# Kernel tuning notes

Hardware: AMD Instinct MI355X
Metric: run time of the kernel (lower is better)

Reference implementation:

```python
import jax, jax.numpy as jnp
import numpy as np

DIM = 1024
H = 16
HD = DIM // H  # 64
B, N = 2, 2048
EPS = 1e-6


def setup_inputs() -> dict:
    key = jax.random.key(0)
    ks = jax.random.split(key, 12)
    s = 0.02
    return {
        "x": jax.random.normal(ks[0], (B, N, DIM), jnp.float32),
        "rotary_cos": jax.random.uniform(ks[1], (B, N, HD), jnp.float32),
        "rotary_sin": jax.random.uniform(ks[2], (B, N, HD), jnp.float32),
        "Wq": jax.random.normal(ks[3], (DIM, DIM), jnp.float32) * s,
        "bq": jnp.zeros((DIM,), jnp.float32),
        "Wk": jax.random.normal(ks[4], (DIM, DIM), jnp.float32) * s,
        "bk": jnp.zeros((DIM,), jnp.float32),
        "Wv": jax.random.normal(ks[5], (DIM, DIM), jnp.float32) * s,
        "bv": jnp.zeros((DIM,), jnp.float32),
        "q_norm_w": jnp.ones((HD,), jnp.float32),
        "q_norm_b": jnp.zeros((HD,), jnp.float32),
        "k_norm_w": jnp.ones((HD,), jnp.float32),
        "k_norm_b": jnp.zeros((HD,), jnp.float32),
        "Wo": jax.random.normal(ks[6], (DIM, DIM), jnp.float32) * s,
        "bo": jnp.zeros((DIM,), jnp.float32),
    }


def _layernorm(x, w, b):
    mu = jnp.mean(x, axis=-1, keepdims=True)
    var = jnp.mean(jnp.square(x - mu), axis=-1, keepdims=True)
    return (x - mu) * jax.lax.rsqrt(var + EPS) * w + b


def _rotate_half(x):
    x1, x2 = jnp.split(x, 2, axis=-1)
    return jnp.concatenate((-x2, x1), axis=-1)


def _apply_rope(x, cos, sin):
    # x: [B,H,N,D]; cos/sin: [B,N,D] -> [B,1,N,D]
    cos = cos[:, None]
    sin = sin[:, None]
    return x * cos + _rotate_half(x) * sin


def reference(x, rotary_cos, rotary_sin, Wq, bq, Wk, bk, Wv, bv,
              q_norm_w, q_norm_b, k_norm_w, k_norm_b, Wo, bo):
    b, n, c = x.shape
    q = x @ Wq + bq
    k = x @ Wk + bk
    v = x @ Wv + bv
    # Faithful packed-qkv permutation: cat -> view(.., H, 3*hd) -> split(hd)
    qkv = jnp.concatenate((q, k, v), axis=-1).reshape(b, n, H, 3 * HD)
    q, k, v = jnp.split(qkv, 3, axis=-1)  # each [B,N,H,HD]
    q = q.transpose(0, 2, 1, 3)  # [B,H,N,HD]
    k = k.transpose(0, 2, 1, 3)
    v = v.transpose(0, 2, 1, 3)
    q = _layernorm(q, q_norm_w, q_norm_b)
    k = _layernorm(k, k_norm_w, k_norm_b)
    q = _apply_rope(q, rotary_cos, rotary_sin)
    k = _apply_rope(k, rotary_cos, rotary_sin)
    scale = HD ** -0.5
    scores = jnp.einsum("bhqd,bhkd->bhqk", q, k) * scale
    probs = jax.nn.softmax(scores, axis=-1)
    out = jnp.einsum("bhqk,bhkd->bhqd", probs, v)
    out = out.transpose(0, 2, 1, 3).reshape(b, n, c)
    return out @ Wo + bo
```

## Files before the change

### kernel.cpp

```cpp
#include <hip/hip_runtime.h>

typedef __attribute__((ext_vector_type(8))) __bf16 bf16x8;
typedef __attribute__((ext_vector_type(4))) float  f32x4;

#define DEV __device__ __forceinline__

DEV void async_copy16(const void* g, void* l) {
  __builtin_amdgcn_global_load_lds((const __attribute__((address_space(1))) void*)g,
                                   (__attribute__((address_space(3))) void*)l, 16, 0, 0);
}

DEV float ldf(const void* p, size_t i, int isbf) {
  if (isbf) {
    unsigned int w = ((unsigned int)((const unsigned short*)p)[i]) << 16;
    float f; __builtin_memcpy(&f, &w, 4); return f;
  }
  return ((const float*)p)[i];
}

__global__ void detect_dtype(const unsigned short* __restrict__ x, int* __restrict__ flag) {
  int bad = 0;
#pragma unroll
  for (int i = 0; i < 4; i++) {
    unsigned short u = x[threadIdx.x + i * 64];
    int e = (u >> 7) & 0xFF;
    if (e >= 0x90) bad = 1;
  }
  int anybad = __any(bad);
  if (threadIdx.x == 0) flag[0] = anybad ? 0 : 1;
}

__global__ __launch_bounds__(256) void prep(const void* __restrict__ Wq,
                                            const void* __restrict__ Wk,
                                            const void* __restrict__ Wv,
                                            const void* __restrict__ Wo,
                                            const void* __restrict__ x,
                                            const void* __restrict__ bq,
                                            const void* __restrict__ bk,
                                            const void* __restrict__ bv,
                                            const void* __restrict__ bo,
                                            const int* __restrict__ flag,
                                            __bf16* __restrict__ Wt,
                                            __bf16* __restrict__ Wot,
                                            __bf16* __restrict__ x_bf,
                                            float* __restrict__ bias) {
  __shared__ float tile[32][33];
  const int isbf = flag[0];
  const int tid = threadIdx.x;
  const int z = blockIdx.z;

  if (z < 4) {
    const void* in = (z == 0) ? Wq : (z == 1) ? Wk : (z == 2) ? Wv : Wo;
    __bf16* out = (z < 3) ? (Wt + (size_t)z * 1024 * 1024) : Wot;
    const int tx = tid & 31, ty = tid >> 5;
    const int r0 = blockIdx.y * 32, c0 = blockIdx.x * 32;
#pragma unroll
    for (int i = 0; i < 4; i++) {
      int r = ty + i * 8;
      tile[r][tx] = ldf(in, (size_t)(r0 + r) * 1024 + c0 + tx, isbf);
    }
    __syncthreads();
#pragma unroll
    for (int i = 0; i < 4; i++) {
      int r = ty + i * 8;
      out[(size_t)(c0 + r) * 1024 + r0 + tx] = (__bf16)tile[tx][r];
    }
  } else {
    const int id = blockIdx.y * 32 + blockIdx.x;
    if (isbf) {
#pragma unroll
      for (int j = 0; j < 4; j++) {
        int idx = id * 1024 + j * 256 + tid;
        ((uint2*)x_bf)[idx] = ((const uint2*)x)[idx];
      }
    } else {
#pragma unroll
      for (int j = 0; j < 4; j++) {
        int idx = id * 1024 + j * 256 + tid;
        float4 f = ((const float4*)x)[idx];
        union { __bf16 h[4]; uint2 u; } pk;
        pk.h[0] = (__bf16)f.x; pk.h[1] = (__bf16)f.y;
        pk.h[2] = (__bf16)f.z; pk.h[3] = (__bf16)f.w;
        ((uint2*)x_bf)[idx] = pk.u;
      }
    }
    if (id < 16) {
      int i = id * 256 + tid;
      if (i < 1024)      bias[i] = ldf(bq, i, isbf);
      else if (i < 2048) bias[i] = ldf(bk, i - 1024, isbf);
      else if (i < 3072) bias[i] = ldf(bv, i - 2048, isbf);
      else               bias[i] = ldf(bo, i - 3072, isbf);
    }
  }
}

template <int DYN>
__global__ __launch_bounds__(256, 2) void gemm_bt(const __bf16* __restrict__ A,
                                                  const __bf16* __restrict__ Bt,
                                                  const float* __restrict__ bias,
                                                  void* __restrict__ Cout,
                                                  const int* __restrict__ flag,
                                                  int M, int N, int K) {
  __shared__ __align__(16) __bf16 As[128 * 64];
  __shared__ __align__(16) __bf16 Bs[128 * 64];
  const int tid = threadIdx.x;
  const int wid = tid >> 6, lane = tid & 63;
  const int m_blk = blockIdx.x * 128, n_blk = blockIdx.y * 128;
  const int wm = (wid & 1) * 64, wn = (wid >> 1) * 64;
  const int l8 = lane >> 3, l7 = lane & 7;
  const int cc = l7 ^ (l8 & 7);
  const int q4 = lane >> 4, l15 = lane & 15;

  f32x4 acc[4][4] = {};

  for (int kb = 0; kb < K; kb += 64) {
    __syncthreads();
#pragma unroll
    for (int i = 0; i < 4; i++) {
      int row = i * 32 + wid * 8 + l8;
      async_copy16(A + (size_t)(m_blk + row) * K + kb + cc * 8,
                   As + (i * 32 + wid * 8) * 64);
      async_copy16(Bt + (size_t)(n_blk + row) * K + kb + cc * 8,
                   Bs + (i * 32 + wid * 8) * 64);
    }
    __syncthreads();
#pragma unroll
    for (int k0 = 0; k0 < 64; k0 += 32) {
      bf16x8 a[4], b[4];
#pragma unroll
      for (int i = 0; i < 4; i++) {
        int ra = wm + i * 16 + l15;
        int ba = ra * 8 + (((k0 >> 3) + q4) ^ (ra & 7));
        a[i] = *(const bf16x8*)&As[ba * 8];
        int rb = wn + i * 16 + l15;
        int bb = rb * 8 + (((k0 >> 3) + q4) ^ (rb & 7));
        b[i] = *(const bf16x8*)&Bs[bb * 8];
      }
#pragma unroll
      for (int i = 0; i < 4; i++)
#pragma unroll
        for (int j = 0; j < 4; j++)
          acc[i][j] = __builtin_amdgcn_mfma_f32_16x16x32_bf16(a[i], b[j], acc[i][j], 0, 0, 0);
    }
  }

  const int isbf = DYN ? flag[0] : 1;
  float bcol[4];
#pragma unroll
  for (int j = 0; j < 4; j++) bcol[j] = bias[n_blk + wn + j * 16 + l15];
#pragma unroll
  for (int i = 0; i < 4; i++)
#pragma unroll
    for (int j = 0; j < 4; j++) {
      int col = n_blk + wn + j * 16 + l15;
#pragma unroll
      for (int r = 0; r < 4; r++) {
        int row = m_blk + wm + i * 16 + q4 * 4 + r;
        float v = acc[i][j][r] + bcol[j];
        size_t idx = (size_t)row * N + col;
        if (isbf) ((__bf16*)Cout)[idx] = (__bf16)v;
        else      ((float*)Cout)[idx] = v;
      }
    }
}

__global__ __launch_bounds__(256) void ln_rope_v(const __bf16* __restrict__ qkv,
                                                 const void* __restrict__ rcos,
                                                 const void* __restrict__ rsin,
                                                 const void* __restrict__ qw,
                                                 const void* __restrict__ qb,
                                                 const void* __restrict__ kw,
                                                 const void* __restrict__ kb_,
                                                 const int* __restrict__ flag,
                                                 __bf16* __restrict__ Qp,
                                                 __bf16* __restrict__ Kp,
                                                 __bf16* __restrict__ Vt) {
  __shared__ __bf16 vt[64][68];
  const int isbf = flag[0];
  const int tid = threadIdx.x, w = tid >> 6, lane = tid & 63;
  const int bh = blockIdx.y, h = bh & 15, b = bh >> 4;
  const int n0 = blockIdx.x * 64;

  float gq = ldf(qw, lane, isbf), bq_ = ldf(qb, lane, isbf);
  float gk = ldf(kw, lane, isbf), bk_ = ldf(kb_, lane, isbf);

  for (int t = 0; t < 16; t++) {
    const int n = n0 + w * 16 + t;
    const size_t tok = (size_t)b * 2048 + n;
    const __bf16* base = qkv + tok * 3072 + h * 192;
    float qv = (float)base[lane], kv = (float)base[64 + lane], vv = (float)base[128 + lane];

    float sq = qv, sk = kv;
#pragma unroll
    for (int m = 1; m < 64; m <<= 1) { sq += __shfl_xor(sq, m, 64); sk += __shfl_xor(sk, m, 64); }
    float muq = sq * (1.0f / 64.0f), muk = sk * (1.0f / 64.0f);
    float tq = qv - muq, tk = kv - muk;
    float vq = tq * tq, vk = tk * tk;
#pragma unroll
    for (int m = 1; m < 64; m <<= 1) { vq += __shfl_xor(vq, m, 64); vk += __shfl_xor(vk, m, 64); }
    float rsq = rsqrtf(vq * (1.0f / 64.0f) + 1e-6f);
    float rsk = rsqrtf(vk * (1.0f / 64.0f) + 1e-6f);
    float qn = tq * rsq * gq + bq_;
    float kn = tk * rsk * gk + bk_;

    float c = ldf(rcos, tok * 64 + lane, isbf), s = ldf(rsin, tok * 64 + lane, isbf);
    float qpart = __shfl_xor(qn, 32, 64), kpart = __shfl_xor(kn, 32, 64);
    float qrh = (lane < 32) ? -qpart : qpart;
    float krh = (lane < 32) ? -kpart : kpart;

    const size_t oidx = ((size_t)bh * 2048 + n) * 64 + lane;
    Qp[oidx] = (__bf16)((qn * c + qrh * s) * 0.1803368801111204f);
    Kp[oidx] = (__bf16)(kn * c + krh * s);
    vt[lane][w * 16 + t] = (__bf16)vv;
  }
  __syncthreads();
  const int row = tid >> 2, qt = tid & 3;
  size_t gbase = (size_t)bh * 64 * 2048 + (size_t)row * 2048 + n0 + qt * 16;
#pragma unroll
  for (int u = 0; u < 4; u++)
    *(uint2*)&Vt[gbase + u * 4] = *(const uint2*)&vt[row][qt * 16 + u * 4];
}

__global__ __launch_bounds__(256, 2) void attn(const __bf16* __restrict__ Qp,
                                               const __bf16* __restrict__ Kp,
                                               const __bf16* __restrict__ Vt,
                                               __bf16* __restrict__ Obuf) {
  __shared__ __align__(16) __bf16 sK[2][4096];
  __shared__ __align__(16) __bf16 sV[2][4096];
  __shared__ __align__(16) __bf16 sP[4][2048];

  const int tid = threadIdx.x, wid = tid >> 6, lane = tid & 63;
  const int q4 = lane >> 4, l15 = lane & 15;
  const int bh = blockIdx.y;
  const int q0w = blockIdx.x * 128 + wid * 32;
  const __bf16* Qb = Qp + (size_t)bh * 2048 * 64;
  const __bf16* Kb = Kp + (size_t)bh * 2048 * 64;
  const __bf16* Vb = Vt + (size_t)bh * 64 * 2048;
  __bf16* sPw = &sP[wid][0];
  const int pbase = (q4 >> 1) * 128 + l15 * 8 + (q4 & 1) * 4;

  bf16x8 qf[2][2];
#pragma unroll
  for (int qs = 0; qs < 2; qs++)
#pragma unroll
    for (int c = 0; c < 2; c++)
      qf[qs][c] = *(const bf16x8*)&Qb[(size_t)(q0w + qs * 16 + l15) * 64 + c * 32 + q4 * 8];

  f32x4 o[2][4] = {};
  float lsum[2] = {0.f, 0.f};

#define STAGE(kt, bf)                                                                   \
  do {                                                                                  \
    async_copy16(Kb + (size_t)((kt) + wid * 16 + l15) * 64 + q4 * 8,                    \
                 &sK[bf][(wid * 2 + 0) * 512]);                                         \
    async_copy16(Kb + (size_t)((kt) + wid * 16 + l15) * 64 + 32 + q4 * 8,               \
                 &sK[bf][(wid * 2 + 1) * 512]);                                         \
    async_copy16(Vb + (size_t)(wid * 16 + l15) * 2048 + (kt) + q4 * 8,                  \
                 &sV[bf][(wid * 2 + 0) * 512]);                                         \
    async_copy16(Vb + (size_t)(wid * 16 + l15) * 2048 + (kt) + 32 + q4 * 8,             \
                 &sV[bf][(wid * 2 + 1) * 512]);                                         \
  } while (0)

  STAGE(0, 0);

  for (int it = 0; it < 32; ++it) {
    const int buf = it & 1;
    __syncthreads();
    if (it < 31) STAGE((it + 1) * 64, buf ^ 1);

    f32x4 sc[2][4];
#pragma unroll
    for (int ks = 0; ks < 4; ks++) {
      bf16x8 ak0 = *(const bf16x8*)&sK[buf][((ks * 2 + 0) * 64 + lane) * 8];
      bf16x8 ak1 = *(const bf16x8*)&sK[buf][((ks * 2 + 1) * 64 + lane) * 8];
#pragma unroll
      for (int qs = 0; qs < 2; qs++) {
        f32x4 z = {0.f, 0.f, 0.f, 0.f};
        z = __builtin_amdgcn_mfma_f32_16x16x32_bf16(ak0, qf[qs][0], z, 0, 0, 0);
        z = __builtin_amdgcn_mfma_f32_16x16x32_bf16(ak1, qf[qs][1], z, 0, 0, 0);
        sc[qs][ks] = z;
      }
    }

#pragma unroll
    for (int qs = 0; qs < 2; qs++)
#pragma unroll
      for (int ks = 0; ks < 4; ks++) {
        union { __bf16 h[4]; uint2 u; } pk;
#pragma unroll
        for (int r = 0; r < 4; r++) {
          float p = exp2f(sc[qs][ks][r]);
          lsum[qs] += p;
          pk.h[r] = (__bf16)p;
        }
        *(uint2*)&sPw[(qs * 2 + (ks >> 1)) * 512 + (ks & 1) * 256 + pbase] = pk.u;
      }
    asm volatile("s_waitcnt lgkmcnt(0)" ::: "memory");

    bf16x8 pb[2][2];
#pragma unroll
    for (int qs = 0; qs < 2; qs++)
#pragma unroll
      for (int c = 0; c < 2; c++)
        pb[qs][c] = *(const bf16x8*)&sPw[((qs * 2 + c) * 64 + lane) * 8];
#pragma unroll
    for (int ds = 0; ds < 4; ds++) {
      bf16x8 av0 = *(const bf16x8*)&sV[buf][((ds * 2 + 0) * 64 + lane) * 8];
      bf16x8 av1 = *(const bf16x8*)&sV[buf][((ds * 2 + 1) * 64 + lane) * 8];
#pragma unroll
      for (int qs = 0; qs < 2; qs++) {
        o[qs][ds] = __builtin_amdgcn_mfma_f32_16x16x32_bf16(av0, pb[qs][0], o[qs][ds], 0, 0, 0);
        o[qs][ds] = __builtin_amdgcn_mfma_f32_16x16x32_bf16(av1, pb[qs][1], o[qs][ds], 0, 0, 0);
      }
    }
  }
#undef STAGE

  const int b = bh >> 4, h = bh & 15;
#pragma unroll
  for (int qs = 0; qs < 2; qs++) {
    float l = lsum[qs];
    l += __shfl_xor(l, 16, 64);
    l += __shfl_xor(l, 32, 64);
    float rl = 1.0f / l;
    size_t base = (size_t)(b * 2048 + q0w + qs * 16 + l15) * 1024 + h * 64;
#pragma unroll
    for (int ds = 0; ds < 4; ds++) {
      union { __bf16 h4[4]; uint2 u; } pk;
#pragma unroll
      for (int r = 0; r < 4; r++) pk.h4[r] = (__bf16)(o[qs][ds][r] * rl);
      *(uint2*)&Obuf[base + ds * 16 + q4 * 4] = pk.u;
    }
  }
}

extern "C" void kernel_launch(void* const* d_in, const int* in_sizes, int n_in,
                              void* d_out, int out_size, void* d_ws, size_t ws_size,
                              hipStream_t stream) {
  const void* x   = d_in[0];
  const void* rc  = d_in[1];
  const void* rs  = d_in[2];
  const void* Wq  = d_in[3];
  const void* bq  = d_in[4];
  const void* Wk  = d_in[5];
  const void* bk  = d_in[6];
  const void* Wv  = d_in[7];
  const void* bv  = d_in[8];
  const void* qnw = d_in[9];
  const void* qnb = d_in[10];
  const void* knw = d_in[11];
  const void* knb = d_in[12];
  const void* Wo  = d_in[13];
  const void* bo  = d_in[14];

  char* ws = (char*)d_ws;
  __bf16* qkv  = (__bf16*)ws;
  __bf16* Obuf = (__bf16*)ws;
  __bf16* Qp   = (__bf16*)(ws + 25165824);
  __bf16* Kp   = (__bf16*)(ws + 33554432);
  __bf16* Vt   = (__bf16*)(ws + 41943040);
  __bf16* Wt   = (__bf16*)(ws + 50331648);
  __bf16* Wot  = (__bf16*)(ws + 56623104);
  float*  bias = (float*)(ws + 58720256);
  __bf16* x_bf = (__bf16*)(ws + 58736640);
  int*    flag = (int*)(ws + 67125248);

  detect_dtype<<<1, 64, 0, stream>>>((const unsigned short*)x, flag);
  prep<<<dim3(32, 32, 5), 256, 0, stream>>>(Wq, Wk, Wv, Wo, x, bq, bk, bv, bo, flag,
                                            Wt, Wot, x_bf, bias);
  gemm_bt<0><<<dim3(32, 24), 256, 0, stream>>>(x_bf, Wt, bias, qkv, flag, 4096, 3072, 1024);
  ln_rope_v<<<dim3(32, 32), 256, 0, stream>>>(qkv, rc, rs, qnw, qnb, knw, knb, flag,
                                              Qp, Kp, Vt);
  attn<<<dim3(16, 32), 256, 0, stream>>>(Qp, Kp, Vt, Obuf);
  gemm_bt<1><<<dim3(32, 8), 256, 0, stream>>>(Obuf, Wot, bias + 3072, d_out, flag,
                                              4096, 1024, 1024);
}
```

Baseline: 247.7 us.

## Inline dtype detection, skip bf16 x copy, triple-buffer attention, narrow output GEMM tiles

Drops the separate dtype-detection kernel: every kernel now recomputes the bf16 check from the first 64 elements of x. When the input is already bf16, prep no longer copies x and the QKV GEMM reads x directly. The attention kernel moves from double to triple buffering for K/V, using explicit vmcnt waits and a raw barrier, and stages Q through LDS. The output projection GEMM uses 64-wide N tiles, doubling its grid to 512 blocks to fill more CUs, at the cost of redundant detection loads in every block and more A-tile traffic.

```diff
diff --git a/kernel.cpp b/kernel.cpp
--- a/kernel.cpp
+++ b/kernel.cpp
@@ -18,16 +18,14 @@
   return ((const float*)p)[i];
 }
 
-__global__ void detect_dtype(const unsigned short* __restrict__ x, int* __restrict__ flag) {
+DEV int detect_isbf(const unsigned short* __restrict__ x) {
   int bad = 0;
 #pragma unroll
-  for (int i = 0; i < 4; i++) {
-    unsigned short u = x[threadIdx.x + i * 64];
-    int e = (u >> 7) & 0xFF;
-    if (e >= 0x90) bad = 1;
-  }
-  int anybad = __any(bad);
-  if (threadIdx.x == 0) flag[0] = anybad ? 0 : 1;
+  for (int i = 0; i < 64; i++) {
+    int e = (x[i] >> 7) & 0xFF;
+    bad |= (e >= 0x90) ? 1 : 0;
+  }
+  return !bad;
 }
 
 __global__ __launch_bounds__(256) void prep(const void* __restrict__ Wq,
@@ -39,13 +37,12 @@
                                             const void* __restrict__ bk,
                                             const void* __restrict__ bv,
                                             const void* __restrict__ bo,
-                                            const int* __restrict__ flag,
                                             __bf16* __restrict__ Wt,
                                             __bf16* __restrict__ Wot,
                                             __bf16* __restrict__ x_bf,
                                             float* __restrict__ bias) {
   __shared__ float tile[32][33];
-  const int isbf = flag[0];
+  const int isbf = detect_isbf((const unsigned short*)x);
   const int tid = threadIdx.x;
   const int z = blockIdx.z;
 
@@ -67,13 +64,7 @@
     }
   } else {
     const int id = blockIdx.y * 32 + blockIdx.x;
-    if (isbf) {
-#pragma unroll
-      for (int j = 0; j < 4; j++) {
-        int idx = id * 1024 + j * 256 + tid;
-        ((uint2*)x_bf)[idx] = ((const uint2*)x)[idx];
-      }
-    } else {
+    if (!isbf) {
 #pragma unroll
       for (int j = 0; j < 4; j++) {
         int idx = id * 1024 + j * 256 + tid;
@@ -94,72 +85,86 @@
   }
 }
 
-template <int DYN>
+template <int DYN, int NT, int ALT>
 __global__ __launch_bounds__(256, 2) void gemm_bt(const __bf16* __restrict__ A,
+                                                  const __bf16* __restrict__ Aalt,
                                                   const __bf16* __restrict__ Bt,
                                                   const float* __restrict__ bias,
                                                   void* __restrict__ Cout,
-                                                  const int* __restrict__ flag,
+                                                  const unsigned short* __restrict__ xdet,
                                                   int M, int N, int K) {
+  constexpr int WN = NT / 2;
+  constexpr int JB = WN / 16;
+  constexpr int NR = NT / 32;
   __shared__ __align__(16) __bf16 As[128 * 64];
-  __shared__ __align__(16) __bf16 Bs[128 * 64];
+  __shared__ __align__(16) __bf16 Bs[NT * 64];
   const int tid = threadIdx.x;
   const int wid = tid >> 6, lane = tid & 63;
-  const int m_blk = blockIdx.x * 128, n_blk = blockIdx.y * 128;
-  const int wm = (wid & 1) * 64, wn = (wid >> 1) * 64;
+  const int m_blk = blockIdx.x * 128, n_blk = blockIdx.y * NT;
+  const int wm = (wid & 1) * 64, wn = (wid >> 1) * WN;
   const int l8 = lane >> 3, l7 = lane & 7;
   const int cc = l7 ^ (l8 & 7);
   const int q4 = lane >> 4, l15 = lane & 15;
 
-  f32x4 acc[4][4] = {};
+  int isbf = 1;
+  if (DYN || ALT) isbf = detect_isbf(xdet);
+  const __bf16* Ap = (ALT && isbf) ? Aalt : A;
+
+  f32x4 acc[4][JB] = {};
 
   for (int kb = 0; kb < K; kb += 64) {
     __syncthreads();
 #pragma unroll
     for (int i = 0; i < 4; i++) {
       int row = i * 32 + wid * 8 + l8;
-      async_copy16(A + (size_t)(m_blk + row) * K + kb + cc * 8,
+      async_copy16(Ap + (size_t)(m_blk + row) * K + kb + cc * 8,
                    As + (i * 32 + wid * 8) * 64);
+    }
+#pragma unroll
+    for (int i = 0; i < NR; i++) {
+      int row = i * 32 + wid * 8 + l8;
       async_copy16(Bt + (size_t)(n_blk + row) * K + kb + cc * 8,
                    Bs + (i * 32 + wid * 8) * 64);
     }
     __syncthreads();
 #pragma unroll
     for (int k0 = 0; k0 < 64; k0 += 32) {
-      bf16x8 a[4], b[4];
+      bf16x8 a[4], b[JB];
 #pragma unroll
       for (int i = 0; i < 4; i++) {
         int ra = wm + i * 16 + l15;
         int ba = ra * 8 + (((k0 >> 3) + q4) ^ (ra & 7));
         a[i] = *(const bf16x8*)&As[ba * 8];
-        int rb = wn + i * 16 + l15;
+      }
+#pragma unroll
+      for (int j = 0; j < JB; j++) {
+        int rb = wn + j * 16 + l15;
         int bb = rb * 8 + (((k0 >> 3) + q4) ^ (rb & 7));
-        b[i] = *(const bf16x8*)&Bs[bb * 8];
+        b[j] = *(const bf16x8*)&Bs[bb * 8];
       }
 #pragma unroll
       for (int i = 0; i < 4; i++)
 #pragma unroll
-        for (int j = 0; j < 4; j++)
+        for (int j = 0; j < JB; j++)
           acc[i][j] = __builtin_amdgcn_mfma_f32_16x16x32_bf16(a[i], b[j], acc[i][j], 0, 0, 0);
     }
   }
 
-  const int isbf = DYN ? flag[0] : 1;
-  float bcol[4];
-#pragma unroll
-  for (int j = 0; j < 4; j++) bcol[j] = bias[n_blk + wn + j * 16 + l15];
+  float bcol[JB];
+#pragma unroll
+  for (int j = 0; j < JB; j++) bcol[j] = bias[n_blk + wn + j * 16 + l15];
 #pragma unroll
   for (int i = 0; i < 4; i++)
 #pragma unroll
-    for (int j = 0; j < 4; j++) {
+    for (int j = 0; j < JB; j++) {
       int col = n_blk + wn + j * 16 + l15;
 #pragma unroll
       for (int r = 0; r < 4; r++) {
         int row = m_blk + wm + i * 16 + q4 * 4 + r;
         float v = acc[i][j][r] + bcol[j];
         size_t idx = (size_t)row * N + col;
-        if (isbf) ((__bf16*)Cout)[idx] = (__bf16)v;
-        else      ((float*)Cout)[idx] = v;
+        if (DYN && !isbf) ((float*)Cout)[idx] = v;
+        else              ((__bf16*)Cout)[idx] = (__bf16)v;
       }
     }
 }
@@ -171,12 +176,12 @@
                                                  const void* __restrict__ qb,
                                                  const void* __restrict__ kw,
                                                  const void* __restrict__ kb_,
-                                                 const int* __restrict__ flag,
+                                                 const unsigned short* __restrict__ xdet,
                                                  __bf16* __restrict__ Qp,
                                                  __bf16* __restrict__ Kp,
                                                  __bf16* __restrict__ Vt) {
   __shared__ __bf16 vt[64][68];
-  const int isbf = flag[0];
+  const int isbf = detect_isbf(xdet);
   const int tid = threadIdx.x, w = tid >> 6, lane = tid & 63;
   const int bh = blockIdx.y, h = bh & 15, b = bh >> 4;
   const int n0 = blockIdx.x * 64;
@@ -225,8 +230,8 @@
                                                const __bf16* __restrict__ Kp,
                                                const __bf16* __restrict__ Vt,
                                                __bf16* __restrict__ Obuf) {
-  __shared__ __align__(16) __bf16 sK[2][4096];
-  __shared__ __align__(16) __bf16 sV[2][4096];
+  __shared__ __align__(16) __bf16 sK[3][4096];
+  __shared__ __align__(16) __bf16 sV[3][4096];
   __shared__ __align__(16) __bf16 sP[4][2048];
 
   const int tid = threadIdx.x, wid = tid >> 6, lane = tid & 63;
@@ -238,16 +243,6 @@
   const __bf16* Vb = Vt + (size_t)bh * 64 * 2048;
   __bf16* sPw = &sP[wid][0];
   const int pbase = (q4 >> 1) * 128 + l15 * 8 + (q4 & 1) * 4;
-
-  bf16x8 qf[2][2];
-#pragma unroll
-  for (int qs = 0; qs < 2; qs++)
-#pragma unroll
-    for (int c = 0; c < 2; c++)
-      qf[qs][c] = *(const bf16x8*)&Qb[(size_t)(q0w + qs * 16 + l15) * 64 + c * 32 + q4 * 8];
-
-  f32x4 o[2][4] = {};
-  float lsum[2] = {0.f, 0.f};
 
 #define STAGE(kt, bf)                                                                   \
   do {                                                                                  \
@@ -261,12 +256,35 @@
                  &sV[bf][(wid * 2 + 1) * 512]);                                         \
   } while (0)
 
+#pragma unroll
+  for (int qs = 0; qs < 2; qs++)
+#pragma unroll
+    for (int c = 0; c < 2; c++)
+      async_copy16(Qb + (size_t)(q0w + qs * 16 + l15) * 64 + c * 32 + q4 * 8,
+                   &sPw[(qs * 2 + c) * 512]);
   STAGE(0, 0);
+  STAGE(64, 1);
+  asm volatile("s_waitcnt vmcnt(8)" ::: "memory");
+
+  bf16x8 qf[2][2];
+#pragma unroll
+  for (int qs = 0; qs < 2; qs++)
+#pragma unroll
+    for (int c = 0; c < 2; c++)
+      qf[qs][c] = *(const bf16x8*)&sPw[((qs * 2 + c) * 64 + lane) * 8];
+
+  f32x4 o[2][4] = {};
+  float lsum[2] = {0.f, 0.f};
+  int buf = 0;
 
   for (int it = 0; it < 32; ++it) {
-    const int buf = it & 1;
-    __syncthreads();
-    if (it < 31) STAGE((it + 1) * 64, buf ^ 1);
+    if (it < 31) asm volatile("s_waitcnt vmcnt(4)" ::: "memory");
+    else         asm volatile("s_waitcnt vmcnt(0)" ::: "memory");
+    asm volatile("s_barrier" ::: "memory");
+    if (it <= 29) {
+      int b2 = buf + 2; if (b2 >= 3) b2 -= 3;
+      STAGE((it + 2) * 64, b2);
+    }
 
     f32x4 sc[2][4];
 #pragma unroll
@@ -313,6 +331,7 @@
         o[qs][ds] = __builtin_amdgcn_mfma_f32_16x16x32_bf16(av1, pb[qs][1], o[qs][ds], 0, 0, 0);
       }
     }
+    buf = (buf == 2) ? 0 : buf + 1;
   }
 #undef STAGE
 
@@ -352,6 +371,7 @@
   const void* knb = d_in[12];
   const void* Wo  = d_in[13];
   const void* bo  = d_in[14];
+  const unsigned short* xdet = (const unsigned short*)x;
 
   char* ws = (char*)d_ws;
   __bf16* qkv  = (__bf16*)ws;
@@ -363,15 +383,14 @@
   __bf16* Wot  = (__bf16*)(ws + 56623104);
   float*  bias = (float*)(ws + 58720256);
   __bf16* x_bf = (__bf16*)(ws + 58736640);
-  int*    flag = (int*)(ws + 67125248);
-
-  detect_dtype<<<1, 64, 0, stream>>>((const unsigned short*)x, flag);
-  prep<<<dim3(32, 32, 5), 256, 0, stream>>>(Wq, Wk, Wv, Wo, x, bq, bk, bv, bo, flag,
+
+  prep<<<dim3(32, 32, 5), 256, 0, stream>>>(Wq, Wk, Wv, Wo, x, bq, bk, bv, bo,
                                             Wt, Wot, x_bf, bias);
-  gemm_bt<0><<<dim3(32, 24), 256, 0, stream>>>(x_bf, Wt, bias, qkv, flag, 4096, 3072, 1024);
-  ln_rope_v<<<dim3(32, 32), 256, 0, stream>>>(qkv, rc, rs, qnw, qnb, knw, knb, flag,
+  gemm_bt<0, 128, 1><<<dim3(32, 24), 256, 0, stream>>>(x_bf, (const __bf16*)x, Wt, bias,
+                                                       qkv, xdet, 4096, 3072, 1024);
+  ln_rope_v<<<dim3(32, 32), 256, 0, stream>>>(qkv, rc, rs, qnw, qnb, knw, knb, xdet,
                                               Qp, Kp, Vt);
   attn<<<dim3(16, 32), 256, 0, stream>>>(Qp, Kp, Vt, Obuf);
-  gemm_bt<1><<<dim3(32, 8), 256, 0, stream>>>(Obuf, Wot, bias + 3072, d_out, flag,
-                                              4096, 1024, 1024);
-}
+  gemm_bt<1, 64, 0><<<dim3(32, 16), 256, 0, stream>>>(Obuf, nullptr, Wot, bias + 3072,
+                                                      d_out, xdet, 4096, 1024, 1024);
+}
```

Result: no change. 247.1 us (-0.2%).
